# Optimization experiments

Hardware: AMD Instinct MI355X
Metric: run time of the kernel (lower is better)

## Reference

```python
import jax, jax.numpy as jnp
import numpy as np

N = 100000
E = 1600000
IN_C, HID, OUT_C = 40, 64, 3


def _glorot(key, shape):
    fan_in, fan_out = shape[1], shape[0]
    lim = float(np.sqrt(6.0 / (fan_in + fan_out)))
    return jax.random.uniform(key, shape, jnp.float32, -lim, lim)


def setup_inputs() -> dict:
    key = jax.random.key(0)
    ks = jax.random.split(key, 12)
    x = jax.random.normal(ks[0], (N, IN_C), dtype=jnp.float32)
    edge_index = jax.random.randint(ks[1], (2, E), 0, N, dtype=jnp.int64)
    # Layer dims: 40->64, 64->128, 128->3. PyG SAGEConv: lin_l (neighbor, with bias), lin_r (root, no bias).
    params = {
        'W1l': _glorot(ks[2], (HID, IN_C)), 'b1': jnp.zeros((HID,), jnp.float32), 'W1r': _glorot(ks[3], (HID, IN_C)),
        'W2l': _glorot(ks[4], (2 * HID, HID)), 'b2': jnp.zeros((2 * HID,), jnp.float32), 'W2r': _glorot(ks[5], (2 * HID, HID)),
        'W4l': _glorot(ks[6], (OUT_C, 2 * HID)), 'b4': jnp.zeros((OUT_C,), jnp.float32), 'W4r': _glorot(ks[7], (OUT_C, 2 * HID)),
    }
    return {'x': x, 'edge_index': edge_index, **params}


def _sage_conv(x, src, dst, deg_inv, Wl, bl, Wr):
    # mean-aggregate neighbor messages x[src] at dst, then lin_l(agg) + lin_r(x) + b
    msgs = x[src]                                            # [E, F]
    agg = jax.ops.segment_sum(msgs, dst, num_segments=N)     # [N, F]
    mean = agg * deg_inv[:, None]
    return mean @ Wl.T + bl + x @ Wr.T


def reference(x, edge_index, W1l, b1, W1r, W2l, b2, W2r, W4l, b4, W4r):
    src, dst = edge_index[0], edge_index[1]
    deg = jax.ops.segment_sum(jnp.ones((E,), x.dtype), dst, num_segments=N)
    deg_inv = jnp.where(deg > 0, 1.0 / jnp.maximum(deg, 1.0), 0.0)
    h = jax.nn.relu(_sage_conv(x, src, dst, deg_inv, W1l, b1, W1r))
    h = jax.nn.relu(_sage_conv(h, src, dst, deg_inv, W2l, b2, W2r))
    h = _sage_conv(h, src, dst, deg_inv, W4l, b4, W4r)
    return h
```

## Files before the change

kernel.cpp:

```cpp
#include <hip/hip_runtime.h>
#include <hip/hip_bf16.h>


static constexpr int NN = 100000;
static constexpr int EE = 1600000;
static constexpr int NRANGE = 256;
static constexpr int RSIZE = (NN + NRANGE - 1) / NRANGE;
static constexpr int RPAD = 512;
static constexpr int NBUCKET = 8 * NRANGE;
static constexpr int CAP = 1024;
static constexpr int BCHUNK = 2048;
static constexpr int BUCKET_BLOCKS = (EE + BCHUNK - 1) / BCHUNK;
static constexpr int CVT_BLOCKS = (NN * 40 / 8 + 255) / 256;
static constexpr int NCHUNK16 = NN / 16;
static constexpr int EIDX = 512;

static constexpr int W1OFF = 0;
static constexpr int W2OFF = 4 * 4 * 64 * 8;
static constexpr int W4OFF = W2OFF + 8 * 4 * 64 * 8;
static constexpr int WPACK_SHORTS = W4OFF + 4 * 64 * 8;
static constexpr int PACK_ITEMS = 4 * 4 * 64 + 8 * 4 * 64 + 4 * 64;
static constexpr int PACK_BLOCKS = (PACK_ITEMS + 255) / 256;

typedef __attribute__((ext_vector_type(8))) short short8;
typedef __attribute__((ext_vector_type(4))) float f32x4;

__device__ __forceinline__ float bf2f(unsigned short u) {
    union { unsigned int i; float f; } c; c.i = ((unsigned int)u) << 16; return c.f;
}
__device__ __forceinline__ unsigned short f2bf(float f) {
    union { float f; unsigned int i; } c; c.f = f;
    unsigned int x = c.i;
    return (unsigned short)((x + 0x7fffu + ((x >> 16) & 1u)) >> 16);
}

__global__ __launch_bounds__(256) void k_bucket_cvt(const int* __restrict__ src, const int* __restrict__ dst,
                                                    int* __restrict__ pcur, unsigned int* __restrict__ pairs,
                                                    const float* __restrict__ x, unsigned short* __restrict__ xb,
                                                    const float* __restrict__ W1l, const float* __restrict__ W1r,
                                                    const float* __restrict__ W2l, const float* __restrict__ W2r,
                                                    const float* __restrict__ W4l, const float* __restrict__ W4r,
                                                    unsigned short* __restrict__ wpack) {
    __shared__ int cnt[NRANGE];
    __shared__ int base[NRANGE];
    const int tid = threadIdx.x;
    if (blockIdx.x >= BUCKET_BLOCKS + CVT_BLOCKS) {
        int idx = (blockIdx.x - BUCKET_BLOCKS - CVT_BLOCKS) * 256 + tid;
        if (idx < PACK_ITEMS) {
            short8 v;
            if (idx < 1024) {
                int l = idx & 63, ks = (idx >> 6) & 3, t = idx >> 8;
                int o = t * 16 + (l & 15);
                int kbase = ks * 32 + (l >> 4) * 8;
#pragma unroll
                for (int j = 0; j < 8; ++j) {
                    int k = kbase + j; float w;
                    if (k < 64) w = (k < 40) ? W1l[o * 40 + k] : 0.f;
                    else { int k2 = k - 64; w = (k2 < 40) ? W1r[o * 40 + k2] : 0.f; }
                    v[j] = (short)f2bf(w);
                }
                *(short8*)&wpack[W1OFF + idx * 8] = v;
            } else if (idx < 3072) {
                int i2 = idx - 1024;
                int l = i2 & 63, ks = (i2 >> 6) & 3, t = i2 >> 8;
                int o = t * 16 + (l & 15);
                int kbase = ks * 32 + (l >> 4) * 8;
#pragma unroll
                for (int j = 0; j < 8; ++j) {
                    int k = kbase + j;
                    float w = (k < 64) ? W2l[o * 64 + k] : W2r[o * 64 + (k - 64)];
                    v[j] = (short)f2bf(w);
                }
                *(short8*)&wpack[W2OFF + i2 * 8] = v;
            } else {
                int i4 = idx - 3072;
                int l = i4 & 63, ks = i4 >> 6;
                int o = l & 15;
                int kbase = ks * 32 + (l >> 4) * 8;
#pragma unroll
                for (int j = 0; j < 8; ++j) {
                    int k = kbase + j;
                    float w = 0.f;
                    if (o < 3) w = W4l[o * 128 + k];
                    else if (o >= 4 && o < 7) w = W4r[(o - 4) * 128 + k];
                    v[j] = (short)f2bf(w);
                }
                *(short8*)&wpack[W4OFF + i4 * 8] = v;
            }
        }
        return;
    }
    if (blockIdx.x >= BUCKET_BLOCKS) {
        int i = (blockIdx.x - BUCKET_BLOCKS) * 256 + tid;
        if (i < NN * 40 / 8) {
            const float4* p = (const float4*)(x + (size_t)i * 8);
            float4 a = p[0], b = p[1];
            short8 v;
            v[0] = (short)f2bf(a.x); v[1] = (short)f2bf(a.y); v[2] = (short)f2bf(a.z); v[3] = (short)f2bf(a.w);
            v[4] = (short)f2bf(b.x); v[5] = (short)f2bf(b.y); v[6] = (short)f2bf(b.z); v[7] = (short)f2bf(b.w);
            *(short8*)(xb + (size_t)i * 8) = v;
        }
        return;
    }
    const int part = blockIdx.x & 7;
    const int e0 = blockIdx.x * BCHUNK;
    cnt[tid] = 0;
    __syncthreads();
    int r_[8], lp_[8];
    unsigned int p_[8];
#pragma unroll
    for (int j = 0; j < 8; ++j) {
        int e = e0 + j * 256 + tid;
        r_[j] = -1;
        if (e < EE) {
            int d = dst[e];
            int s = src[e];
            int r = d / RSIZE;
            r_[j] = r;
            p_[j] = (unsigned int)s | ((unsigned int)(d - r * RSIZE) << 17);
            lp_[j] = atomicAdd(&cnt[r], 1);
        }
    }
    __syncthreads();
    {
        int c = cnt[tid];
        base[tid] = (c > 0) ? atomicAdd(&pcur[(part << 8) | tid], c) : 0;
    }
    __syncthreads();
#pragma unroll
    for (int j = 0; j < 8; ++j) {
        if (r_[j] >= 0) {
            int pos = base[r_[j]] + lp_[j];
            if (pos < CAP) pairs[(size_t)((part << 8) | r_[j]) * CAP + pos] = p_[j];
        }
    }
}

__global__ __launch_bounds__(1024) void k_build(const unsigned int* __restrict__ pairs,
                                                const int* __restrict__ pcur,
                                                int* __restrict__ row_start, float* __restrict__ deg_inv,
                                                int* __restrict__ csr_src) {
    __shared__ int ldeg[RPAD];
    __shared__ int lrs[RPAD];
    __shared__ int rtot[NRANGE];
    const int tid = threadIdx.x;
    const int r = blockIdx.x;
    const int lo = r * RSIZE;
    const int nloc = (lo + RSIZE <= NN) ? RSIZE : (NN - lo);
    for (int t = tid; t < RPAD; t += 1024) ldeg[t] = 0;
    __syncthreads();
    for (int p = 0; p < 8; ++p) {
        int b = (p << 8) | r;
        int len = pcur[b]; if (len > CAP) len = CAP;
        const unsigned int* bp = pairs + (size_t)b * CAP;
        for (int i = tid; i < len; i += 1024)
            atomicAdd(&ldeg[bp[i] >> 17], 1);
    }
    if (tid < NRANGE) {
        int s = 0;
#pragma unroll
        for (int p = 0; p < 8; ++p) {
            int c = pcur[(p << 8) | tid];
            s += (c > CAP) ? CAP : c;
        }
        rtot[tid] = s;
    }
    __syncthreads();
    for (int d = 1; d < NRANGE; d <<= 1) {
        int t = (tid < NRANGE && tid >= d) ? rtot[tid - d] : 0;
        __syncthreads();
        if (tid < NRANGE) rtot[tid] += t;
        __syncthreads();
    }
    const int rbase = (r == 0) ? 0 : rtot[r - 1];
    if (tid < RPAD) lrs[tid] = ldeg[tid];
    __syncthreads();
    for (int d = 1; d < RPAD; d <<= 1) {
        int t = (tid < RPAD && tid >= d) ? lrs[tid - d] : 0;
        __syncthreads();
        if (tid < RPAD) lrs[tid] += t;
        __syncthreads();
    }
    int excl = 0, dg = 0;
    if (tid < RPAD) { dg = ldeg[tid]; excl = lrs[tid] - dg; }
    if (tid < nloc) {
        row_start[lo + tid] = rbase + excl;
        deg_inv[lo + tid] = (dg > 0) ? 1.0f / (float)dg : 0.0f;
    }
    if (r == 0 && tid == 0) row_start[NN] = EE;
    __syncthreads();
    if (tid < RPAD) { lrs[tid] = excl; ldeg[tid] = 0; }
    __syncthreads();
    for (int p = 0; p < 8; ++p) {
        int b = (p << 8) | r;
        int len = pcur[b]; if (len > CAP) len = CAP;
        const unsigned int* bp = pairs + (size_t)b * CAP;
        for (int i = tid; i < len; i += 1024) {
            unsigned int pk = bp[i];
            int dloc = pk >> 17;
            int lp = atomicAdd(&ldeg[dloc], 1);
            csr_src[rbase + lrs[dloc] + lp] = (int)(pk & 0x1FFFFu);
        }
    }
}

template<int Fin, int Fout, bool RELU, bool ZR, int WOFF>
__global__ __launch_bounds__(128) void k_fused(const unsigned short* __restrict__ xin,
                                               const int* __restrict__ row_start,
                                               const int* __restrict__ csr_src,
                                               const float* __restrict__ deg_inv,
                                               const unsigned short* __restrict__ wpack,
                                               const float* __restrict__ bias,
                                               unsigned short* __restrict__ out,
                                               float* __restrict__ z,
                                               float* __restrict__ rr_) {
    constexpr int KS = 4;
    constexpr int TILES = Fout / 16;
    constexpr int TPW = TILES / 2;
    constexpr int SMEAN = 0;
    constexpr int SROOT = 16 * 72;
    constexpr int SH2 = 2 * 16 * 72;
    constexpr int SHM = 2 * 16 * 72 + (ZR ? 16 * 136 : 0);
    __shared__ short shm[SHM];
    __shared__ int lidx[EIDX];
    const int tid = threadIdx.x;
    const int lane = tid & 63;
    const int wv = tid >> 6;
    const int nbase = blockIdx.x * 16;

    float bias_t[TPW];
#pragma unroll
    for (int tt = 0; tt < TPW; ++tt) bias_t[tt] = bias[(wv * TPW + tt) * 16 + (lane & 15)];

    const int rs_blk = row_start[nbase];
    const int re_blk = row_start[nbase + 16];
    const int nedge = re_blk - rs_blk;
    for (int i = tid; i < nedge && i < EIDX; i += 128) lidx[i] = csr_src[rs_blk + i];
    __syncthreads();

    const int node8 = tid >> 3;
    const int c = tid & 7;

    {
        const int node = nbase + node8;
        float acc[8] = {0, 0, 0, 0, 0, 0, 0, 0};
        short8 rv = {0, 0, 0, 0, 0, 0, 0, 0};
        if (c * 8 < Fin) {
            const unsigned short* xq = xin + c * 8;
            const int rs = row_start[node], re = row_start[node + 1];
            int k = rs;
            for (; k + 8 <= re; k += 8) {
                short8 v[8];
#pragma unroll
                for (int j = 0; j < 8; ++j) {
                    int off = k + j - rs_blk;
                    int s = (off < EIDX) ? lidx[off] : csr_src[k + j];
                    v[j] = *(const short8*)(xq + (size_t)s * Fin);
                }
#pragma unroll
                for (int j = 0; j < 8; ++j)
#pragma unroll
                    for (int t = 0; t < 8; ++t) acc[t] += bf2f((unsigned short)v[j][t]);
            }
            if (k < re) {
                short8 v[8];
#pragma unroll
                for (int j = 0; j < 8; ++j) {
                    int kk = (k + j < re) ? (k + j) : (re - 1);
                    int off = kk - rs_blk;
                    int s = (off < EIDX) ? lidx[off] : csr_src[kk];
                    v[j] = *(const short8*)(xq + (size_t)s * Fin);
                }
#pragma unroll
                for (int j = 0; j < 8; ++j) {
                    float m = (k + j < re) ? 1.f : 0.f;
#pragma unroll
                    for (int t = 0; t < 8; ++t) acc[t] += m * bf2f((unsigned short)v[j][t]);
                }
            }
            float di = deg_inv[node];
#pragma unroll
            for (int t = 0; t < 8; ++t) acc[t] *= di;
            rv = *(const short8*)(xin + (size_t)node * Fin + c * 8);
        }
        short8 mv;
#pragma unroll
        for (int t = 0; t < 8; ++t) mv[t] = (c * 8 < Fin) ? (short)f2bf(acc[t]) : (short)0;
        *(short8*)&shm[SMEAN + node8 * 72 + c * 8] = mv;
        *(short8*)&shm[SROOT + node8 * 72 + c * 8] = rv;
    }
    __syncthreads();
    short8 af[KS];
#pragma unroll
    for (int ks = 0; ks < KS; ++ks) {
        const int base = (ks < 2) ? SMEAN : SROOT;
        const int g = (ks & 1) * 4 + (lane >> 4);
        af[ks] = *(const short8*)&shm[base + (lane & 15) * 72 + g * 8];
    }
    f32x4 acc2[TPW];
#pragma unroll
    for (int tt = 0; tt < TPW; ++tt) acc2[tt] = (f32x4){0.f, 0.f, 0.f, 0.f};
#pragma unroll
    for (int tt = 0; tt < TPW; ++tt) {
        short8 bt[KS];
#pragma unroll
        for (int ks = 0; ks < KS; ++ks)
            bt[ks] = *(const short8*)&wpack[WOFF + (((wv * TPW + tt) * KS + ks) * 64 + lane) * 8];
#pragma unroll
        for (int ks = 0; ks < KS; ++ks)
            acc2[tt] = __builtin_amdgcn_mfma_f32_16x16x32_bf16(af[ks], bt[ks], acc2[tt], 0, 0, 0);
    }
    if constexpr (!ZR) {
        const int nrow = nbase + (lane >> 4) * 4;
#pragma unroll
        for (int tt = 0; tt < TPW; ++tt) {
            int col = (wv * TPW + tt) * 16 + (lane & 15);
#pragma unroll
            for (int q = 0; q < 4; ++q) {
                float v = acc2[tt][q] + bias_t[tt];
                if (RELU) v = fmaxf(v, 0.f);
                out[(size_t)(nrow + q) * Fout + col] = f2bf(v);
            }
        }
    } else {
        const int row0 = (lane >> 4) * 4;
#pragma unroll
        for (int tt = 0; tt < TPW; ++tt) {
            int col = (wv * TPW + tt) * 16 + (lane & 15);
#pragma unroll
            for (int q = 0; q < 4; ++q) {
                float v = acc2[tt][q] + bias_t[tt];
                if (RELU) v = fmaxf(v, 0.f);
                shm[SH2 + (row0 + q) * 136 + col] = (short)f2bf(v);
            }
        }
        __syncthreads();
        if (wv == 0) {
            short8 b4r[4];
#pragma unroll
            for (int ks = 0; ks < 4; ++ks)
                b4r[ks] = *(const short8*)&wpack[W4OFF + (ks * 64 + lane) * 8];
            const int row = lane & 15;
            f32x4 az = (f32x4){0.f, 0.f, 0.f, 0.f};
#pragma unroll
            for (int ks = 0; ks < 4; ++ks) {
                short8 a4 = *(const short8*)&shm[SH2 + row * 136 + (ks * 4 + (lane >> 4)) * 8];
                az = __builtin_amdgcn_mfma_f32_16x16x32_bf16(a4, b4r[ks], az, 0, 0, 0);
            }
            const int col = lane & 15;
            const int nr = nbase + (lane >> 4) * 4;
            if (col < 3) {
#pragma unroll
                for (int q = 0; q < 4; ++q) z[(size_t)(nr + q) * 4 + col] = az[q];
            } else if (col >= 4 && col < 7) {
#pragma unroll
                for (int q = 0; q < 4; ++q) rr_[(size_t)(nr + q) * 4 + col - 4] = az[q];
            }
        }
    }
}

__global__ __launch_bounds__(256) void k_final(const float* __restrict__ z, const float* __restrict__ r,
                                               const float* __restrict__ b4,
                                               const int* __restrict__ row_start, const int* __restrict__ csr_src,
                                               const float* __restrict__ deg_inv, float* __restrict__ out) {
    int n = blockIdx.x * 256 + threadIdx.x;
    if (n >= NN) return;
    const int rs = row_start[n], re = row_start[n + 1];
    float a0 = 0, a1 = 0, a2 = 0, b0 = 0, b1 = 0, b2 = 0;
    const float4* z4 = (const float4*)z;
    int k = rs;
    for (; k + 8 <= re; k += 8) {
        int e[8];
#pragma unroll
        for (int j = 0; j < 8; ++j) e[j] = csr_src[k + j];
        float4 v[8];
#pragma unroll
        for (int j = 0; j < 8; ++j) v[j] = z4[e[j]];
#pragma unroll
        for (int j = 0; j < 8; j += 2) {
            a0 += v[j].x; a1 += v[j].y; a2 += v[j].z;
            b0 += v[j + 1].x; b1 += v[j + 1].y; b2 += v[j + 1].z;
        }
    }
    if (k < re) {
        int e[8];
#pragma unroll
        for (int j = 0; j < 8; ++j) e[j] = csr_src[(k + j < re) ? (k + j) : (re - 1)];
        float4 v[8];
#pragma unroll
        for (int j = 0; j < 8; ++j) v[j] = z4[e[j]];
#pragma unroll
        for (int j = 0; j < 8; ++j) {
            float m = (k + j < re) ? 1.f : 0.f;
            a0 += m * v[j].x; a1 += m * v[j].y; a2 += m * v[j].z;
        }
    }
    float di = deg_inv[n];
    float4 rn = *(const float4*)&r[4 * (size_t)n];
    out[(size_t)n * 3 + 0] = (a0 + b0) * di + rn.x + b4[0];
    out[(size_t)n * 3 + 1] = (a1 + b1) * di + rn.y + b4[1];
    out[(size_t)n * 3 + 2] = (a2 + b2) * di + rn.z + b4[2];
}

extern "C" void kernel_launch(void* const* d_in, const int* in_sizes, int n_in,
                              void* d_out, int out_size, void* d_ws, size_t ws_size,
                              hipStream_t stream) {
    const float* x   = (const float*)d_in[0];
    const int*   ei  = (const int*)d_in[1];
    const float* W1l = (const float*)d_in[2];
    const float* b1  = (const float*)d_in[3];
    const float* W1r = (const float*)d_in[4];
    const float* W2l = (const float*)d_in[5];
    const float* b2  = (const float*)d_in[6];
    const float* W2r = (const float*)d_in[7];
    const float* W4l = (const float*)d_in[8];
    const float* b4  = (const float*)d_in[9];
    const float* W4r = (const float*)d_in[10];
    float* out = (float*)d_out;

    char* ws = (char*)d_ws;
    size_t off = 0;
    auto alloc = [&](size_t bytes) -> void* {
        void* p = ws + off;
        off = (off + bytes + 255) & ~(size_t)255;
        return p;
    };
    int*   row_start = (int*)alloc(((size_t)NN + 1) * 4);
    int*   csr_src   = (int*)alloc((size_t)EE * 4);
    float* deg_inv   = (float*)alloc((size_t)NN * 4);
    int*   pcur      = (int*)alloc((size_t)NBUCKET * 4);
    unsigned short* xb    = (unsigned short*)alloc((size_t)NN * 40 * 2);
    unsigned short* h1    = (unsigned short*)alloc((size_t)NN * 64 * 2);
    unsigned short* wpack = (unsigned short*)alloc((size_t)WPACK_SHORTS * 2);
    float* zbuf = (float*)alloc((size_t)NN * 4 * 4);
    float* rbuf = (float*)alloc((size_t)NN * 4 * 4);
    unsigned int* pairs = (unsigned int*)alloc((size_t)NBUCKET * CAP * 4);

    const int* e_src = ei;
    const int* e_dst = ei + EE;

    hipMemsetAsync(pcur, 0, (size_t)NBUCKET * 4, stream);

    k_bucket_cvt<<<BUCKET_BLOCKS + CVT_BLOCKS + PACK_BLOCKS, 256, 0, stream>>>(
        e_src, e_dst, pcur, pairs, x, xb, W1l, W1r, W2l, W2r, W4l, W4r, wpack);
    k_build<<<NRANGE, 1024, 0, stream>>>(pairs, pcur, row_start, deg_inv, csr_src);

    k_fused<40, 64, true, false, W1OFF><<<NCHUNK16, 128, 0, stream>>>(
        xb, row_start, csr_src, deg_inv, wpack, b1, h1, nullptr, nullptr);
    k_fused<64, 128, true, true, W2OFF><<<NCHUNK16, 128, 0, stream>>>(
        h1, row_start, csr_src, deg_inv, wpack, b2, nullptr, zbuf, rbuf);
    k_final<<<(NN + 255) / 256, 256, 0, stream>>>(zbuf, rbuf, b4, row_start, csr_src, deg_inv, out);
}
```

Baseline: 197.5 us.

## Sub-bucket edges by source range and pad layer-1 features to 64

Edge bucketing now splits each destination range into 16 source-range sub-buckets, so the CSR neighbour list of each node comes out ordered by source range. That should improve locality of the feature gathers in the aggregation kernels. Per-range totals are accumulated with atomics during bucketing instead of being recomputed in the build kernel. The bf16 input features are padded from 40 to 64 columns so both fused layers share one 64-wide gather path. This costs more memory traffic for the padded features and many more buckets. The per-bucket capacity of 128 could overflow on skewed inputs.

```diff
diff --git a/kernel.cpp b/kernel.cpp
--- a/kernel.cpp
+++ b/kernel.cpp
@@ -7,11 +7,13 @@
 static constexpr int NRANGE = 256;
 static constexpr int RSIZE = (NN + NRANGE - 1) / NRANGE;
 static constexpr int RPAD = 512;
-static constexpr int NBUCKET = 8 * NRANGE;
-static constexpr int CAP = 1024;
+static constexpr int SRN = 16;
+static constexpr int SRSZ = NN / SRN;
+static constexpr int NBUCKET2 = 8 * NRANGE * SRN;
+static constexpr int CAP2 = 128;
 static constexpr int BCHUNK = 2048;
 static constexpr int BUCKET_BLOCKS = (EE + BCHUNK - 1) / BCHUNK;
-static constexpr int CVT_BLOCKS = (NN * 40 / 8 + 255) / 256;
+static constexpr int CVT_BLOCKS = (NN * 64 / 8 + 255) / 256;
 static constexpr int NCHUNK16 = NN / 16;
 static constexpr int EIDX = 512;
 
@@ -35,14 +37,16 @@
 }
 
 __global__ __launch_bounds__(256) void k_bucket_cvt(const int* __restrict__ src, const int* __restrict__ dst,
-                                                    int* __restrict__ pcur, unsigned int* __restrict__ pairs,
+                                                    int* __restrict__ pcur, int* __restrict__ drtot,
+                                                    unsigned int* __restrict__ pairs,
                                                     const float* __restrict__ x, unsigned short* __restrict__ xb,
                                                     const float* __restrict__ W1l, const float* __restrict__ W1r,
                                                     const float* __restrict__ W2l, const float* __restrict__ W2r,
                                                     const float* __restrict__ W4l, const float* __restrict__ W4r,
                                                     unsigned short* __restrict__ wpack) {
-    __shared__ int cnt[NRANGE];
-    __shared__ int base[NRANGE];
+    __shared__ int cnt[NRANGE * SRN];
+    __shared__ int base[NRANGE * SRN];
+    __shared__ int drc[NRANGE];
     const int tid = threadIdx.x;
     if (blockIdx.x >= BUCKET_BLOCKS + CVT_BLOCKS) {
         int idx = (blockIdx.x - BUCKET_BLOCKS - CVT_BLOCKS) * 256 + tid;
@@ -92,52 +96,67 @@
     }
     if (blockIdx.x >= BUCKET_BLOCKS) {
         int i = (blockIdx.x - BUCKET_BLOCKS) * 256 + tid;
-        if (i < NN * 40 / 8) {
-            const float4* p = (const float4*)(x + (size_t)i * 8);
-            float4 a = p[0], b = p[1];
-            short8 v;
-            v[0] = (short)f2bf(a.x); v[1] = (short)f2bf(a.y); v[2] = (short)f2bf(a.z); v[3] = (short)f2bf(a.w);
-            v[4] = (short)f2bf(b.x); v[5] = (short)f2bf(b.y); v[6] = (short)f2bf(b.z); v[7] = (short)f2bf(b.w);
+        if (i < NN * 8) {
+            int node = i >> 3, c = i & 7;
+            short8 v = {0, 0, 0, 0, 0, 0, 0, 0};
+            if (c < 5) {
+                const float4* p = (const float4*)(x + (size_t)node * 40 + c * 8);
+                float4 a = p[0], b = p[1];
+                v[0] = (short)f2bf(a.x); v[1] = (short)f2bf(a.y); v[2] = (short)f2bf(a.z); v[3] = (short)f2bf(a.w);
+                v[4] = (short)f2bf(b.x); v[5] = (short)f2bf(b.y); v[6] = (short)f2bf(b.z); v[7] = (short)f2bf(b.w);
+            }
             *(short8*)(xb + (size_t)i * 8) = v;
         }
         return;
     }
     const int part = blockIdx.x & 7;
     const int e0 = blockIdx.x * BCHUNK;
-    cnt[tid] = 0;
-    __syncthreads();
-    int r_[8], lp_[8];
+#pragma unroll
+    for (int j = 0; j < SRN; ++j) cnt[j * 256 + tid] = 0;
+    if (tid < NRANGE) drc[tid] = 0;
+    __syncthreads();
+    int key_[8], lp_[8];
     unsigned int p_[8];
 #pragma unroll
     for (int j = 0; j < 8; ++j) {
         int e = e0 + j * 256 + tid;
-        r_[j] = -1;
+        key_[j] = -1;
         if (e < EE) {
             int d = dst[e];
             int s = src[e];
-            int r = d / RSIZE;
-            r_[j] = r;
-            p_[j] = (unsigned int)s | ((unsigned int)(d - r * RSIZE) << 17);
-            lp_[j] = atomicAdd(&cnt[r], 1);
-        }
-    }
-    __syncthreads();
-    {
-        int c = cnt[tid];
-        base[tid] = (c > 0) ? atomicAdd(&pcur[(part << 8) | tid], c) : 0;
-    }
-    __syncthreads();
+            int dr = d / RSIZE;
+            int sr = s / SRSZ;
+            key_[j] = (dr << 4) | sr;
+            p_[j] = (unsigned int)s | ((unsigned int)(d - dr * RSIZE) << 17);
+            lp_[j] = atomicAdd(&cnt[key_[j]], 1);
+        }
+    }
+    __syncthreads();
+#pragma unroll
+    for (int j = 0; j < SRN; ++j) {
+        int idx = j * 256 + tid;
+        int c = cnt[idx];
+        int b = 0;
+        if (c > 0) {
+            atomicAdd(&drc[idx >> 4], c);
+            b = atomicAdd(&pcur[(part << 12) | idx], c);
+        }
+        base[idx] = b;
+    }
+    __syncthreads();
+    if (tid < NRANGE && drc[tid] > 0) atomicAdd(&drtot[tid], drc[tid]);
 #pragma unroll
     for (int j = 0; j < 8; ++j) {
-        if (r_[j] >= 0) {
-            int pos = base[r_[j]] + lp_[j];
-            if (pos < CAP) pairs[(size_t)((part << 8) | r_[j]) * CAP + pos] = p_[j];
+        if (key_[j] >= 0) {
+            int pos = base[key_[j]] + lp_[j];
+            if (pos < CAP2) pairs[(size_t)((part << 12) | key_[j]) * CAP2 + pos] = p_[j];
         }
     }
 }
 
 __global__ __launch_bounds__(1024) void k_build(const unsigned int* __restrict__ pairs,
                                                 const int* __restrict__ pcur,
+                                                const int* __restrict__ drtot,
                                                 int* __restrict__ row_start, float* __restrict__ deg_inv,
                                                 int* __restrict__ csr_src) {
     __shared__ int ldeg[RPAD];
@@ -148,23 +167,16 @@
     const int lo = r * RSIZE;
     const int nloc = (lo + RSIZE <= NN) ? RSIZE : (NN - lo);
     for (int t = tid; t < RPAD; t += 1024) ldeg[t] = 0;
-    __syncthreads();
-    for (int p = 0; p < 8; ++p) {
-        int b = (p << 8) | r;
-        int len = pcur[b]; if (len > CAP) len = CAP;
-        const unsigned int* bp = pairs + (size_t)b * CAP;
-        for (int i = tid; i < len; i += 1024)
-            atomicAdd(&ldeg[bp[i] >> 17], 1);
-    }
-    if (tid < NRANGE) {
-        int s = 0;
-#pragma unroll
+    if (tid < NRANGE) rtot[tid] = drtot[tid];
+    __syncthreads();
+    for (int sr = 0; sr < SRN; ++sr)
         for (int p = 0; p < 8; ++p) {
-            int c = pcur[(p << 8) | tid];
-            s += (c > CAP) ? CAP : c;
-        }
-        rtot[tid] = s;
-    }
+            int b = (p << 12) | (r << 4) | sr;
+            int len = pcur[b]; if (len > CAP2) len = CAP2;
+            const unsigned int* bp = pairs + (size_t)b * CAP2;
+            for (int i = tid; i < len; i += 1024)
+                atomicAdd(&ldeg[bp[i] >> 17], 1);
+        }
     __syncthreads();
     for (int d = 1; d < NRANGE; d <<= 1) {
         int t = (tid < NRANGE && tid >= d) ? rtot[tid - d] : 0;
@@ -191,20 +203,21 @@
     __syncthreads();
     if (tid < RPAD) { lrs[tid] = excl; ldeg[tid] = 0; }
     __syncthreads();
-    for (int p = 0; p < 8; ++p) {
-        int b = (p << 8) | r;
-        int len = pcur[b]; if (len > CAP) len = CAP;
-        const unsigned int* bp = pairs + (size_t)b * CAP;
-        for (int i = tid; i < len; i += 1024) {
-            unsigned int pk = bp[i];
-            int dloc = pk >> 17;
-            int lp = atomicAdd(&ldeg[dloc], 1);
-            csr_src[rbase + lrs[dloc] + lp] = (int)(pk & 0x1FFFFu);
-        }
-    }
-}
-
-template<int Fin, int Fout, bool RELU, bool ZR, int WOFF>
+    for (int sr = 0; sr < SRN; ++sr)
+        for (int p = 0; p < 8; ++p) {
+            int b = (p << 12) | (r << 4) | sr;
+            int len = pcur[b]; if (len > CAP2) len = CAP2;
+            const unsigned int* bp = pairs + (size_t)b * CAP2;
+            for (int i = tid; i < len; i += 1024) {
+                unsigned int pk = bp[i];
+                int dloc = pk >> 17;
+                int lp = atomicAdd(&ldeg[dloc], 1);
+                csr_src[rbase + lrs[dloc] + lp] = (int)(pk & 0x1FFFFu);
+            }
+        }
+}
+
+template<int Fout, bool RELU, bool ZR, int WOFF>
 __global__ __launch_bounds__(128) void k_fused(const unsigned short* __restrict__ xin,
                                                const int* __restrict__ row_start,
                                                const int* __restrict__ csr_src,
@@ -244,48 +257,43 @@
     {
         const int node = nbase + node8;
         float acc[8] = {0, 0, 0, 0, 0, 0, 0, 0};
-        short8 rv = {0, 0, 0, 0, 0, 0, 0, 0};
-        if (c * 8 < Fin) {
-            const unsigned short* xq = xin + c * 8;
-            const int rs = row_start[node], re = row_start[node + 1];
-            int k = rs;
-            for (; k + 8 <= re; k += 8) {
-                short8 v[8];
-#pragma unroll
-                for (int j = 0; j < 8; ++j) {
-                    int off = k + j - rs_blk;
-                    int s = (off < EIDX) ? lidx[off] : csr_src[k + j];
-                    v[j] = *(const short8*)(xq + (size_t)s * Fin);
-                }
-#pragma unroll
-                for (int j = 0; j < 8; ++j)
-#pragma unroll
-                    for (int t = 0; t < 8; ++t) acc[t] += bf2f((unsigned short)v[j][t]);
-            }
-            if (k < re) {
-                short8 v[8];
-#pragma unroll
-                for (int j = 0; j < 8; ++j) {
-                    int kk = (k + j < re) ? (k + j) : (re - 1);
-                    int off = kk - rs_blk;
-                    int s = (off < EIDX) ? lidx[off] : csr_src[kk];
-                    v[j] = *(const short8*)(xq + (size_t)s * Fin);
-                }
-#pragma unroll
-                for (int j = 0; j < 8; ++j) {
-                    float m = (k + j < re) ? 1.f : 0.f;
-#pragma unroll
-                    for (int t = 0; t < 8; ++t) acc[t] += m * bf2f((unsigned short)v[j][t]);
-                }
-            }
-            float di = deg_inv[node];
-#pragma unroll
-            for (int t = 0; t < 8; ++t) acc[t] *= di;
-            rv = *(const short8*)(xin + (size_t)node * Fin + c * 8);
-        }
+        const unsigned short* xq = xin + c * 8;
+        const int rs = row_start[node], re = row_start[node + 1];
+        int k = rs;
+        for (; k + 8 <= re; k += 8) {
+            short8 v[8];
+#pragma unroll
+            for (int j = 0; j < 8; ++j) {
+                int off = k + j - rs_blk;
+                int s = (off < EIDX) ? lidx[off] : csr_src[k + j];
+                v[j] = *(const short8*)(xq + (size_t)s * 64);
+            }
+#pragma unroll
+            for (int j = 0; j < 8; ++j)
+#pragma unroll
+                for (int t = 0; t < 8; ++t) acc[t] += bf2f((unsigned short)v[j][t]);
+        }
+        if (k < re) {
+            short8 v[8];
+#pragma unroll
+            for (int j = 0; j < 8; ++j) {
+                int kk = (k + j < re) ? (k + j) : (re - 1);
+                int off = kk - rs_blk;
+                int s = (off < EIDX) ? lidx[off] : csr_src[kk];
+                v[j] = *(const short8*)(xq + (size_t)s * 64);
+            }
+#pragma unroll
+            for (int j = 0; j < 8; ++j) {
+                float m = (k + j < re) ? 1.f : 0.f;
+#pragma unroll
+                for (int t = 0; t < 8; ++t) acc[t] += m * bf2f((unsigned short)v[j][t]);
+            }
+        }
+        float di = deg_inv[node];
         short8 mv;
 #pragma unroll
-        for (int t = 0; t < 8; ++t) mv[t] = (c * 8 < Fin) ? (short)f2bf(acc[t]) : (short)0;
+        for (int t = 0; t < 8; ++t) mv[t] = (short)f2bf(acc[t] * di);
+        short8 rv = *(const short8*)(xin + (size_t)node * 64 + c * 8);
         *(short8*)&shm[SMEAN + node8 * 72 + c * 8] = mv;
         *(short8*)&shm[SROOT + node8 * 72 + c * 8] = rv;
     }
@@ -429,26 +437,27 @@
     int*   row_start = (int*)alloc(((size_t)NN + 1) * 4);
     int*   csr_src   = (int*)alloc((size_t)EE * 4);
     float* deg_inv   = (float*)alloc((size_t)NN * 4);
-    int*   pcur      = (int*)alloc((size_t)NBUCKET * 4);
-    unsigned short* xb    = (unsigned short*)alloc((size_t)NN * 40 * 2);
+    int*   pcur      = (int*)alloc((size_t)(NBUCKET2 + NRANGE) * 4);
+    int*   drtot     = pcur + NBUCKET2;
+    unsigned short* xb    = (unsigned short*)alloc((size_t)NN * 64 * 2);
     unsigned short* h1    = (unsigned short*)alloc((size_t)NN * 64 * 2);
     unsigned short* wpack = (unsigned short*)alloc((size_t)WPACK_SHORTS * 2);
     float* zbuf = (float*)alloc((size_t)NN * 4 * 4);
     float* rbuf = (float*)alloc((size_t)NN * 4 * 4);
-    unsigned int* pairs = (unsigned int*)alloc((size_t)NBUCKET * CAP * 4);
+    unsigned int* pairs = (unsigned int*)alloc((size_t)NBUCKET2 * CAP2 * 4);
 
     const int* e_src = ei;
     const int* e_dst = ei + EE;
 
-    hipMemsetAsync(pcur, 0, (size_t)NBUCKET * 4, stream);
+    hipMemsetAsync(pcur, 0, (size_t)(NBUCKET2 + NRANGE) * 4, stream);
 
     k_bucket_cvt<<<BUCKET_BLOCKS + CVT_BLOCKS + PACK_BLOCKS, 256, 0, stream>>>(
-        e_src, e_dst, pcur, pairs, x, xb, W1l, W1r, W2l, W2r, W4l, W4r, wpack);
-    k_build<<<NRANGE, 1024, 0, stream>>>(pairs, pcur, row_start, deg_inv, csr_src);
-
-    k_fused<40, 64, true, false, W1OFF><<<NCHUNK16, 128, 0, stream>>>(
+        e_src, e_dst, pcur, drtot, pairs, x, xb, W1l, W1r, W2l, W2r, W4l, W4r, wpack);
+    k_build<<<NRANGE, 1024, 0, stream>>>(pairs, pcur, drtot, row_start, deg_inv, csr_src);
+
+    k_fused<64, true, false, W1OFF><<<NCHUNK16, 128, 0, stream>>>(
         xb, row_start, csr_src, deg_inv, wpack, b1, h1, nullptr, nullptr);
-    k_fused<64, 128, true, true, W2OFF><<<NCHUNK16, 128, 0, stream>>>(
+    k_fused<128, true, true, W2OFF><<<NCHUNK16, 128, 0, stream>>>(
         h1, row_start, csr_src, deg_inv, wpack, b2, nullptr, zbuf, rbuf);
     k_final<<<(NN + 255) / 256, 256, 0, stream>>>(zbuf, rbuf, b4, row_start, csr_src, deg_inv, out);
 }
```

Measured after the change: 277.1 us. 40.3% more time.
